# Kernel tuning notes

Hardware: AMD Instinct MI355X
Metric: run time of the kernel (lower is better)

## Reference

```python
import jax, jax.numpy as jnp
import numpy as np

N, E, H, C, G = 10000, 20000, 12, 768, 64  # nodes, edges, heads, per-head dim, graphs
NEG_SLOPE = 0.2


def _gat_layer(x, W, a_src, a_dst, b, src, dst):
    # x: [N, 768], W: [768, H*C], a_src/a_dst: [H, C], b: [C]
    h = (x @ W).reshape(-1, H, C)                      # [N, H, C]
    s = jnp.einsum('nhc,hc->nh', h, a_src)             # alpha_src per node
    d = jnp.einsum('nhc,hc->nh', h, a_dst)             # alpha_dst per node
    e = jax.nn.leaky_relu(s[src] + d[dst], NEG_SLOPE)  # [Etot, H]
    # segment softmax over incoming edges of each destination node
    m = jax.lax.stop_gradient(jax.ops.segment_max(e, dst, num_segments=N))
    ex = jnp.exp(e - m[dst])
    den = jax.ops.segment_sum(ex, dst, num_segments=N)
    alpha = ex / (den[dst] + 1e-16)                    # [Etot, H]
    out = jax.ops.segment_sum(h[src] * alpha[:, :, None], dst, num_segments=N)
    return out.mean(axis=1) + b                        # concat=False -> head mean, [N, C]


def setup_inputs() -> dict:
    key = jax.random.key(0)
    ks = jax.random.split(key, 16)
    sc = 0.02
    f32 = jnp.float32
    return {
        'x': jax.random.normal(ks[0], (N, 768), f32),
        'edge_index': jax.random.randint(ks[1], (2, E), 0, N),
        'batch': jnp.sort(jax.random.randint(ks[2], (N,), 0, G)),
        'W1': (jax.random.normal(ks[3], (768, H * C), f32) * sc),
        'a_src1': (jax.random.normal(ks[4], (H, C), f32) * sc),
        'a_dst1': (jax.random.normal(ks[5], (H, C), f32) * sc),
        'b1': jnp.zeros((C,), f32),
        'W2': (jax.random.normal(ks[6], (768, H * C), f32) * sc),
        'a_src2': (jax.random.normal(ks[7], (H, C), f32) * sc),
        'a_dst2': (jax.random.normal(ks[8], (H, C), f32) * sc),
        'b2': jnp.zeros((C,), f32),
        'mlp_w1': (jax.random.normal(ks[9], (768, 128), f32) * sc),
        'mlp_b1': jnp.zeros((128,), f32),
        'mlp_w2': (jax.random.normal(ks[10], (128, 4), f32) * sc),
        'mlp_b2': jnp.zeros((4,), f32),
    }


def reference(x, edge_index, batch, W1, a_src1, a_dst1, b1, W2, a_src2, a_dst2, b2,
              mlp_w1, mlp_b1, mlp_w2, mlp_b2):
    loops = jnp.arange(N)                               # GATConv add_self_loops=True
    src = jnp.concatenate([edge_index[0], loops])
    dst = jnp.concatenate([edge_index[1], loops])
    h = _gat_layer(x, W1, a_src1, a_dst1, b1, src, dst)
    h = _gat_layer(h, W2, a_src2, a_dst2, b2, src, dst)
    # scatter_mean over graph assignment
    ssum = jax.ops.segment_sum(h, batch, num_segments=G)
    cnt = jax.ops.segment_sum(jnp.ones((N,), h.dtype), batch, num_segments=G)
    g = ssum / jnp.maximum(cnt, 1.0)[:, None]           # [G, 768]
    z = jax.nn.relu(g @ mlp_w1 + mlp_b1)
    return z @ mlp_w2 + mlp_b2                          # [G, 4] logits
```

## Files before the change

### kernel.cpp

```cpp
#include <hip/hip_runtime.h>
#include <stdint.h>

typedef unsigned short u16;
typedef unsigned int   u32;

#define NNODES 10000
#define NEDGES 20000
#define ETOT   30000
#define NHEADS 12
#define CDIM   768
#define FDIM   768
#define KDIM   9216
#define NGRAPH 64
#define MPAD   10240
#define NEG_SLOPE 0.2f
#define DMAX   32

typedef __attribute__((ext_vector_type(8))) short short8;
typedef __attribute__((ext_vector_type(4))) float f32x4;

__device__ __forceinline__ u16 f32_bf16(float f) {
  u32 u = __float_as_uint(f);
  u = (u + 0x7FFFu + ((u >> 16) & 1u)) >> 16;
  return (u16)u;
}
__device__ __forceinline__ float bf16_f32(u16 v) {
  return __uint_as_float(((u32)v) << 16);
}

__global__ void k_count(const int* __restrict__ dste, int* __restrict__ counts) {
  int e = blockIdx.x * blockDim.x + threadIdx.x;
  if (e >= ETOT) return;
  int dst;
  if (e < NEDGES) dst = dste[e]; else dst = e - NEDGES;
  atomicAdd(&counts[dst], 1);
}

__global__ void k_scan(const int* __restrict__ counts, int* __restrict__ offs) {
  __shared__ int part[256];
  int t = threadIdx.x;
  const int chunk = 40;
  int beg = t * chunk;
  int end = beg + chunk; if (end > NNODES) end = NNODES;
  int s = 0;
  for (int i = beg; i < end && i < NNODES; i++) s += counts[i];
  part[t] = s;
  __syncthreads();
  for (int d = 1; d < 256; d <<= 1) {
    int v = (t >= d) ? part[t - d] : 0;
    __syncthreads();
    part[t] += v;
    __syncthreads();
  }
  int base = (t == 0) ? 0 : part[t - 1];
  for (int i = beg; i < end && i < NNODES; i++) { offs[i] = base; base += counts[i]; }
  if (t == 255) offs[NNODES] = base;
}

__global__ void k_seed(const int* __restrict__ offs, int* __restrict__ cursor) {
  int n = blockIdx.x * blockDim.x + threadIdx.x;
  if (n < NNODES) cursor[n] = offs[n];
}

__global__ void k_scatter(const int* __restrict__ dste, int* __restrict__ cursor,
                          int* __restrict__ elist) {
  int e = blockIdx.x * blockDim.x + threadIdx.x;
  if (e >= ETOT) return;
  int dst;
  if (e < NEDGES) dst = dste[e]; else dst = e - NEDGES;
  int pos = atomicAdd(&cursor[dst], 1);
  elist[pos] = e;
}

__global__ void k_U(const float* __restrict__ W, const float* __restrict__ a_src,
                    const float* __restrict__ a_dst, float* __restrict__ Ut) {
  int k = blockIdx.x;
  int t = threadIdx.x, w = t >> 6, l = t & 63;
  const float* Wrow = W + (size_t)k * KDIM;
#pragma unroll
  for (int q = 0; q < 6; q++) {
    int o = w * 6 + q;
    int h = (o < 12) ? o : o - 12;
    const float* av = (o < 12) ? (a_src + h * CDIM) : (a_dst + h * CDIM);
    const float* wr = Wrow + h * CDIM;
    float p = 0.f;
    for (int c = l; c < CDIM; c += 64) p += wr[c] * av[c];
#pragma unroll
    for (int d = 32; d > 0; d >>= 1) p += __shfl_down(p, d, 64);
    if (l == 0) Ut[o * FDIM + k] = p;
  }
}

__global__ void k_sd(const float* __restrict__ xin, const float* __restrict__ Ut,
                     float* __restrict__ sd, u16* __restrict__ xbf) {
  __shared__ float UtS[24 * FDIM];
  int t = threadIdx.x, w = t >> 6, l = t & 63;
  const float4* U4 = (const float4*)Ut;
  float4* S4 = (float4*)UtS;
  for (int i = t; i < 24 * FDIM / 4; i += 256) S4[i] = U4[i];
  __syncthreads();
#pragma unroll
  for (int rep = 0; rep < 5; rep++) {
    int n = blockIdx.x * 20 + w * 5 + rep;
    if (n >= NNODES) continue;
    const float* xr = xin + (size_t)n * FDIM;
    float4 x0 = *(const float4*)(xr + 4 * l);
    float4 x1 = *(const float4*)(xr + 4 * l + 256);
    float4 x2 = *(const float4*)(xr + 4 * l + 512);
    u16* xb = xbf + (size_t)n * FDIM + 4 * l;
    ushort4 p0, p1, p2;
    p0.x = f32_bf16(x0.x); p0.y = f32_bf16(x0.y); p0.z = f32_bf16(x0.z); p0.w = f32_bf16(x0.w);
    p1.x = f32_bf16(x1.x); p1.y = f32_bf16(x1.y); p1.z = f32_bf16(x1.z); p1.w = f32_bf16(x1.w);
    p2.x = f32_bf16(x2.x); p2.y = f32_bf16(x2.y); p2.z = f32_bf16(x2.z); p2.w = f32_bf16(x2.w);
    *(ushort4*)xb = p0;
    *(ushort4*)(xb + 256) = p1;
    *(ushort4*)(xb + 512) = p2;
#pragma unroll
    for (int o = 0; o < 24; o++) {
      const float4* up = (const float4*)(UtS + o * FDIM + 4 * l);
      float4 u0 = up[0];
      float4 u1 = up[64];
      float4 u2 = up[128];
      float a = x0.x * u0.x + x0.y * u0.y + x0.z * u0.z + x0.w * u0.w
              + x1.x * u1.x + x1.y * u1.y + x1.z * u1.z + x1.w * u1.w
              + x2.x * u2.x + x2.y * u2.y + x2.z * u2.z + x2.w * u2.w;
#pragma unroll
      for (int d = 32; d > 0; d >>= 1) a += __shfl_xor(a, d, 64);
      if (l == 0) sd[n * 24 + o] = a;
    }
  }
}

__global__ void k_trans(const float* __restrict__ W, u16* __restrict__ Bt) {
  int kt = blockIdx.x * 32, jt = blockIdx.y * 32;
  int tx = threadIdx.x, ty = threadIdx.y;
  __shared__ float tile[32][33];
#pragma unroll
  for (int r = 0; r < 4; r++)
    tile[ty + 8 * r][tx] = W[(size_t)(kt + ty + 8 * r) * KDIM + jt + tx];
  __syncthreads();
#pragma unroll
  for (int r = 0; r < 4; r++)
    Bt[(size_t)(jt + ty + 8 * r) * FDIM + kt + tx] = f32_bf16(tile[tx][ty + 8 * r]);
}

#define GLL16(G, L) __builtin_amdgcn_global_load_lds( \
  (const __attribute__((address_space(1))) void*)(G), \
  (__attribute__((address_space(3))) void*)(L), 16, 0, 0)

__global__ __launch_bounds__(512, 2) void k_gemm(const u16* __restrict__ A,
    const u16* __restrict__ B, u16* __restrict__ C) {
  __shared__ __align__(16) u16 As[2][256 * 64];
  __shared__ __align__(16) u16 Bs[2][256 * 64];
  int t = threadIdx.x;
  int w = t >> 6, l = t & 63;
  int swz = (blockIdx.x & 7) * 180 + (blockIdx.x >> 3);
  int by = swz / 36, bx = swz - by * 36;
  int row0 = by * 256, col0 = bx * 256;
  int wr = w >> 2, wc = w & 3;
  int lr = l & 15;
  int koff = (l >> 4) * 16;
  int swzr = (lr & 7) << 4;
  int rb = t >> 3;
  int csw = ((t & 7) ^ (rb & 7)) * 8;
  const u16* baseA = A + (size_t)(row0 + rb) * FDIM + csw;
  const u16* baseB = B + (size_t)(col0 + rb) * FDIM + csw;

  f32x4 acc[8][4] = {};
  short8 a[4][2], b0[2][2], b1[2][2];

  auto stA = [&](int buf, int h, int s) {
    const u16* g = baseA + (size_t)(h * 128) * FDIM + s * 64;
    u16* lp = (u16*)&As[buf][0] + h * 8192 + (w << 9);
    GLL16(g, lp);
    GLL16(g + (size_t)64 * FDIM, lp + 4096);
  };
  auto stB = [&](int buf, int h, int s) {
    const u16* g = baseB + (size_t)(h * 128) * FDIM + s * 64;
    u16* lp = (u16*)&Bs[buf][0] + h * 8192 + (w << 9);
    GLL16(g, lp);
    GLL16(g + (size_t)64 * FDIM, lp + 4096);
  };
  auto ldA = [&](int buf, int mo) {
#pragma unroll
    for (int m = 0; m < 4; m++)
#pragma unroll
      for (int c = 0; c < 2; c++) {
        int row = wr * 128 + (mo + m) * 16 + lr;
        int off = row * 128 + ((c * 64 + koff) ^ swzr);
        a[m][c] = *(const short8*)((const char*)&As[buf][0] + off);
      }
  };
  auto ldB = [&](int buf, short8 (*bb)[2], int no) {
#pragma unroll
    for (int n = 0; n < 2; n++)
#pragma unroll
      for (int c = 0; c < 2; c++) {
        int row = wc * 64 + (no + n) * 16 + lr;
        int off = row * 128 + ((c * 64 + koff) ^ swzr);
        bb[n][c] = *(const short8*)((const char*)&Bs[buf][0] + off);
      }
  };
  auto mm8 = [&](short8 (*bb)[2], int mo, int no) {
    __builtin_amdgcn_s_setprio(1);
#pragma unroll
    for (int m = 0; m < 4; m++)
#pragma unroll
      for (int n = 0; n < 2; n++)
#pragma unroll
        for (int c = 0; c < 2; c++)
          acc[mo + m][no + n] = __builtin_amdgcn_mfma_f32_16x16x32_bf16(
              a[m][c], bb[n][c], acc[mo + m][no + n], 0, 0, 0);
    __builtin_amdgcn_s_setprio(0);
  };

  stA(0, 0, 0); stA(0, 1, 0); stB(0, 0, 0); stB(0, 1, 0);
  stB(1, 0, 1); stA(1, 0, 1);
  asm volatile("s_waitcnt vmcnt(4)" ::: "memory");
  __builtin_amdgcn_s_barrier();

#pragma unroll
  for (int s = 0; s < 12; s++) {
    int P = s & 1;
    ldA(P, 0); ldB(P, b0, 0);
    if (s + 1 < 12) stB(P ^ 1, 1, s + 1);
    __builtin_amdgcn_s_barrier();
    mm8(b0, 0, 0);
    __builtin_amdgcn_s_barrier();
    ldB(P, b1, 2);
    if (s + 1 < 12) stA(P ^ 1, 1, s + 1);
    __builtin_amdgcn_s_barrier();
    mm8(b1, 0, 2);
    __builtin_amdgcn_s_barrier();
    ldA(P, 4);
    if (s + 2 < 12) stB(P, 0, s + 2);
    __builtin_amdgcn_s_barrier();
    mm8(b1, 4, 2);
    __builtin_amdgcn_s_barrier();
    if (s + 2 < 12) stA(P, 0, s + 2);
    __builtin_amdgcn_s_barrier();
    mm8(b0, 4, 0);
    if (s < 11) {
      if (s <= 9) asm volatile("s_waitcnt vmcnt(4)" ::: "memory");
      else        asm volatile("s_waitcnt vmcnt(0)" ::: "memory");
    }
    __builtin_amdgcn_s_barrier();
  }

  int lg = l >> 4;
#pragma unroll
  for (int m = 0; m < 8; m++)
#pragma unroll
    for (int n = 0; n < 4; n++) {
      int col = col0 + wc * 64 + n * 16 + lr;
#pragma unroll
      for (int r = 0; r < 4; r++) {
        int row = row0 + wr * 128 + m * 16 + lg * 4 + r;
        C[(size_t)row * KDIM + col] = f32_bf16(acc[m][n][r]);
      }
    }
}

__global__ void k_att(const u16* __restrict__ Hbig, const int* __restrict__ ei,
                      const int* __restrict__ offs, const int* __restrict__ elist,
                      const float* __restrict__ sd, const float* __restrict__ bias,
                      float* __restrict__ out) {
  int t = threadIdx.x, w = t >> 6, l = t & 63;
  int n = blockIdx.x * 4 + w;
  __shared__ int   srcsS[4][DMAX];
  __shared__ float alphS[4][NHEADS * DMAX];
  if (n >= NNODES) return;
  int* srcs = srcsS[w];
  float* alph = alphS[w];
  int beg = offs[n];
  int deg = offs[n + 1] - beg;
  if (deg > DMAX) deg = DMAX;
  if (l < deg) {
    int e = elist[beg + l];
    srcs[l] = (e < NEDGES) ? ei[e] : e - NEDGES;
  }
  __builtin_amdgcn_wave_barrier();
  for (int p = l; p < deg * NHEADS; p += 64) {
    int i = p / NHEADS, h = p - i * NHEADS;
    float v = sd[srcs[i] * 24 + h] + sd[n * 24 + 12 + h];
    v = (v > 0.f) ? v : NEG_SLOPE * v;
    alph[h * DMAX + i] = v;
  }
  __builtin_amdgcn_wave_barrier();
  if (l < NHEADS) {
    float m = -1e30f;
    for (int i = 0; i < deg; i++) m = fmaxf(m, alph[l * DMAX + i]);
    float s = 0.f;
    for (int i = 0; i < deg; i++) {
      float ex = expf(alph[l * DMAX + i] - m);
      alph[l * DMAX + i] = ex;
      s += ex;
    }
    float inv = 1.f / (s + 1e-16f);
    for (int i = 0; i < deg; i++) alph[l * DMAX + i] *= inv;
  }
  __builtin_amdgcn_wave_barrier();
#pragma unroll
  for (int pass = 0; pass < 3; pass++) {
    float4 acc = make_float4(0.f, 0.f, 0.f, 0.f);
    for (int i = 0; i < deg; i++) {
      const u16* hb = Hbig + (size_t)srcs[i] * KDIM + pass * 256 + 4 * l;
#pragma unroll
      for (int h = 0; h < NHEADS; h++) {
        ushort4 hv = *(const ushort4*)(hb + h * CDIM);
        float a = alph[h * DMAX + i];
        acc.x += a * bf16_f32(hv.x);
        acc.y += a * bf16_f32(hv.y);
        acc.z += a * bf16_f32(hv.z);
        acc.w += a * bf16_f32(hv.w);
      }
    }
    int c = pass * 256 + 4 * l;
    const float sc = 1.f / 12.f;
    float4 ov;
    ov.x = acc.x * sc + bias[c + 0];
    ov.y = acc.y * sc + bias[c + 1];
    ov.z = acc.z * sc + bias[c + 2];
    ov.w = acc.w * sc + bias[c + 3];
    *(float4*)(out + (size_t)n * FDIM + c) = ov;
  }
}

__global__ void k_pool(const float* __restrict__ h2, const int* __restrict__ batch,
                       float* __restrict__ g) {
  int gi = blockIdx.x;
  int c = blockIdx.y * 256 + threadIdx.x;
  int lo = 0, hi = NNODES;
  while (lo < hi) { int mid = (lo + hi) >> 1; if (batch[mid] < gi) lo = mid + 1; else hi = mid; }
  int start = lo;
  lo = start; hi = NNODES;
  while (lo < hi) { int mid = (lo + hi) >> 1; if (batch[mid] < gi + 1) lo = mid + 1; else hi = mid; }
  int end = lo;
  int cnt = end - start; if (cnt < 1) cnt = 1;
  float inv = 1.f / (float)cnt;
  float s = 0.f;
  for (int n = start; n < end; n++) s += h2[(size_t)n * FDIM + c];
  g[gi * FDIM + c] = s * inv;
}

__global__ void k_mlp(const float* __restrict__ g, const float* __restrict__ w1,
                      const float* __restrict__ b1, const float* __restrict__ w2,
                      const float* __restrict__ b2, float* __restrict__ out) {
  int gi = blockIdx.x;
  int t = threadIdx.x;
  __shared__ float gs[FDIM];
  __shared__ float zs[128];
  for (int i = t; i < FDIM; i += 128) gs[i] = g[gi * FDIM + i];
  __syncthreads();
  float a = b1[t];
  for (int k = 0; k < FDIM; k++) a += gs[k] * w1[k * 128 + t];
  zs[t] = (a > 0.f) ? a : 0.f;
  __syncthreads();
  if (t < 4) {
    float o = b2[t];
    for (int i = 0; i < 128; i++) o += zs[i] * w2[i * 4 + t];
    out[gi * 4 + t] = o;
  }
}

extern "C" void kernel_launch(void* const* d_in, const int* in_sizes, int n_in,
                              void* d_out, int out_size, void* d_ws, size_t ws_size,
                              hipStream_t stream) {
  const float* x    = (const float*)d_in[0];
  const int*   ei   = (const int*)d_in[1];
  const int*   batch= (const int*)d_in[2];
  const float* W1   = (const float*)d_in[3];
  const float* as1  = (const float*)d_in[4];
  const float* ad1  = (const float*)d_in[5];
  const float* b1   = (const float*)d_in[6];
  const float* W2   = (const float*)d_in[7];
  const float* as2  = (const float*)d_in[8];
  const float* ad2  = (const float*)d_in[9];
  const float* b2   = (const float*)d_in[10];
  const float* mw1  = (const float*)d_in[11];
  const float* mb1  = (const float*)d_in[12];
  const float* mw2  = (const float*)d_in[13];
  const float* mb2  = (const float*)d_in[14];
  float* out = (float*)d_out;
  (void)in_sizes; (void)n_in; (void)out_size; (void)ws_size;

  char* wsb = (char*)d_ws;
  size_t off = 0;
  auto alloc = [&](size_t bytes) -> void* {
    void* p = wsb + off;
    off += (bytes + 255) & ~(size_t)255;
    return p;
  };
  u16*  Hbig   = (u16*)alloc((size_t)MPAD * KDIM * 2);
  u16*  Bt     = (u16*)alloc((size_t)KDIM * FDIM * 2);
  float* h1    = (float*)alloc((size_t)NNODES * FDIM * 4);
  float* h2    = (float*)alloc((size_t)NNODES * FDIM * 4);
  u16*  xbf    = (u16*)h2;
  float* sd    = (float*)alloc((size_t)NNODES * 24 * 4);
  float* Ut    = (float*)alloc((size_t)FDIM * 24 * 4);
  int*  counts = (int*)alloc((size_t)NNODES * 4);
  int*  offs   = (int*)alloc((size_t)(NNODES + 1) * 4);
  int*  cursor = (int*)alloc((size_t)NNODES * 4);
  int*  elist  = (int*)alloc((size_t)ETOT * 4);
  float* gbuf  = (float*)alloc((size_t)NGRAPH * FDIM * 4);

  hipMemsetAsync(counts, 0, NNODES * 4, stream);
  hipMemsetAsync(xbf + (size_t)NNODES * FDIM, 0, (size_t)(MPAD - NNODES) * FDIM * 2, stream);
  k_count<<<(ETOT + 255) / 256, 256, 0, stream>>>(ei + NEDGES, counts);
  k_scan<<<1, 256, 0, stream>>>(counts, offs);
  k_seed<<<(NNODES + 255) / 256, 256, 0, stream>>>(offs, cursor);
  k_scatter<<<(ETOT + 255) / 256, 256, 0, stream>>>(ei + NEDGES, cursor, elist);

  for (int layer = 0; layer < 2; layer++) {
    const float* xin  = layer ? h1  : x;
    const float* W    = layer ? W2  : W1;
    const float* asrc = layer ? as2 : as1;
    const float* adst = layer ? ad2 : ad1;
    const float* bb   = layer ? b2  : b1;
    float* hout       = layer ? h2  : h1;

    k_U<<<FDIM, 256, 0, stream>>>(W, asrc, adst, Ut);
    k_sd<<<(NNODES + 19) / 20, 256, 0, stream>>>(xin, Ut, sd, xbf);
    k_trans<<<dim3(FDIM / 32, KDIM / 32), dim3(32, 8), 0, stream>>>(W, Bt);
    k_gemm<<<dim3((MPAD / 256) * (KDIM / 256)), 512, 0, stream>>>(xbf, Bt, Hbig);
    k_att<<<(NNODES + 3) / 4, 256, 0, stream>>>(Hbig, ei, offs, elist, sd, bb, hout);
  }

  k_pool<<<dim3(NGRAPH, 3), 256, 0, stream>>>(h2, batch, gbuf);
  k_mlp<<<NGRAPH, 128, 0, stream>>>(gbuf, mw1, mb1, mw2, mb2, out);
}
```

Before: 907.7 us.

## Aggregate raw features per head before projection, then GEMM with head-mean fused

The layer is reordered so that attention-weighted aggregation runs on the input features per head, producing a [N, 12*768] bf16 tensor, and the projection comes afterwards. The projection becomes one GEMM with K=9216 against a reshaped weight that sums over heads, and it fuses the 1/12 scale and the bias into its epilogue. This replaces the N×9216 output GEMM and the gather over the large H tensor with a 768-wide output. It relies on linearity and trades a larger bf16 intermediate write for less gather traffic and fewer output columns.

After: 876.9 us. 3.4% less time.

```diff
diff --git a/kernel.cpp b/kernel.cpp
--- a/kernel.cpp
+++ b/kernel.cpp
@@ -92,7 +92,7 @@
 }
 
 __global__ void k_sd(const float* __restrict__ xin, const float* __restrict__ Ut,
-                     float* __restrict__ sd, u16* __restrict__ xbf) {
+                     float* __restrict__ sd) {
   __shared__ float UtS[24 * FDIM];
   int t = threadIdx.x, w = t >> 6, l = t & 63;
   const float4* U4 = (const float4*)Ut;
@@ -107,14 +107,6 @@
     float4 x0 = *(const float4*)(xr + 4 * l);
     float4 x1 = *(const float4*)(xr + 4 * l + 256);
     float4 x2 = *(const float4*)(xr + 4 * l + 512);
-    u16* xb = xbf + (size_t)n * FDIM + 4 * l;
-    ushort4 p0, p1, p2;
-    p0.x = f32_bf16(x0.x); p0.y = f32_bf16(x0.y); p0.z = f32_bf16(x0.z); p0.w = f32_bf16(x0.w);
-    p1.x = f32_bf16(x1.x); p1.y = f32_bf16(x1.y); p1.z = f32_bf16(x1.z); p1.w = f32_bf16(x1.w);
-    p2.x = f32_bf16(x2.x); p2.y = f32_bf16(x2.y); p2.z = f32_bf16(x2.z); p2.w = f32_bf16(x2.w);
-    *(ushort4*)xb = p0;
-    *(ushort4*)(xb + 256) = p1;
-    *(ushort4*)(xb + 512) = p2;
 #pragma unroll
     for (int o = 0; o < 24; o++) {
       const float4* up = (const float4*)(UtS + o * FDIM + 4 * l);
@@ -131,140 +123,23 @@
   }
 }
 
-__global__ void k_trans(const float* __restrict__ W, u16* __restrict__ Bt) {
+__global__ void k_trans2(const float* __restrict__ W, u16* __restrict__ Bt2) {
   int kt = blockIdx.x * 32, jt = blockIdx.y * 32;
   int tx = threadIdx.x, ty = threadIdx.y;
   __shared__ float tile[32][33];
+  int h0 = jt / 768, c0 = jt - h0 * 768;
 #pragma unroll
   for (int r = 0; r < 4; r++)
     tile[ty + 8 * r][tx] = W[(size_t)(kt + ty + 8 * r) * KDIM + jt + tx];
   __syncthreads();
 #pragma unroll
   for (int r = 0; r < 4; r++)
-    Bt[(size_t)(jt + ty + 8 * r) * FDIM + kt + tx] = f32_bf16(tile[tx][ty + 8 * r]);
-}
-
-#define GLL16(G, L) __builtin_amdgcn_global_load_lds( \
-  (const __attribute__((address_space(1))) void*)(G), \
-  (__attribute__((address_space(3))) void*)(L), 16, 0, 0)
-
-__global__ __launch_bounds__(512, 2) void k_gemm(const u16* __restrict__ A,
-    const u16* __restrict__ B, u16* __restrict__ C) {
-  __shared__ __align__(16) u16 As[2][256 * 64];
-  __shared__ __align__(16) u16 Bs[2][256 * 64];
-  int t = threadIdx.x;
-  int w = t >> 6, l = t & 63;
-  int swz = (blockIdx.x & 7) * 180 + (blockIdx.x >> 3);
-  int by = swz / 36, bx = swz - by * 36;
-  int row0 = by * 256, col0 = bx * 256;
-  int wr = w >> 2, wc = w & 3;
-  int lr = l & 15;
-  int koff = (l >> 4) * 16;
-  int swzr = (lr & 7) << 4;
-  int rb = t >> 3;
-  int csw = ((t & 7) ^ (rb & 7)) * 8;
-  const u16* baseA = A + (size_t)(row0 + rb) * FDIM + csw;
-  const u16* baseB = B + (size_t)(col0 + rb) * FDIM + csw;
-
-  f32x4 acc[8][4] = {};
-  short8 a[4][2], b0[2][2], b1[2][2];
-
-  auto stA = [&](int buf, int h, int s) {
-    const u16* g = baseA + (size_t)(h * 128) * FDIM + s * 64;
-    u16* lp = (u16*)&As[buf][0] + h * 8192 + (w << 9);
-    GLL16(g, lp);
-    GLL16(g + (size_t)64 * FDIM, lp + 4096);
-  };
-  auto stB = [&](int buf, int h, int s) {
-    const u16* g = baseB + (size_t)(h * 128) * FDIM + s * 64;
-    u16* lp = (u16*)&Bs[buf][0] + h * 8192 + (w << 9);
-    GLL16(g, lp);
-    GLL16(g + (size_t)64 * FDIM, lp + 4096);
-  };
-  auto ldA = [&](int buf, int mo) {
-#pragma unroll
-    for (int m = 0; m < 4; m++)
-#pragma unroll
-      for (int c = 0; c < 2; c++) {
-        int row = wr * 128 + (mo + m) * 16 + lr;
-        int off = row * 128 + ((c * 64 + koff) ^ swzr);
-        a[m][c] = *(const short8*)((const char*)&As[buf][0] + off);
-      }
-  };
-  auto ldB = [&](int buf, short8 (*bb)[2], int no) {
-#pragma unroll
-    for (int n = 0; n < 2; n++)
-#pragma unroll
-      for (int c = 0; c < 2; c++) {
-        int row = wc * 64 + (no + n) * 16 + lr;
-        int off = row * 128 + ((c * 64 + koff) ^ swzr);
-        bb[n][c] = *(const short8*)((const char*)&Bs[buf][0] + off);
-      }
-  };
-  auto mm8 = [&](short8 (*bb)[2], int mo, int no) {
-    __builtin_amdgcn_s_setprio(1);
-#pragma unroll
-    for (int m = 0; m < 4; m++)
-#pragma unroll
-      for (int n = 0; n < 2; n++)
-#pragma unroll
-        for (int c = 0; c < 2; c++)
-          acc[mo + m][no + n] = __builtin_amdgcn_mfma_f32_16x16x32_bf16(
-              a[m][c], bb[n][c], acc[mo + m][no + n], 0, 0, 0);
-    __builtin_amdgcn_s_setprio(0);
-  };
-
-  stA(0, 0, 0); stA(0, 1, 0); stB(0, 0, 0); stB(0, 1, 0);
-  stB(1, 0, 1); stA(1, 0, 1);
-  asm volatile("s_waitcnt vmcnt(4)" ::: "memory");
-  __builtin_amdgcn_s_barrier();
-
-#pragma unroll
-  for (int s = 0; s < 12; s++) {
-    int P = s & 1;
-    ldA(P, 0); ldB(P, b0, 0);
-    if (s + 1 < 12) stB(P ^ 1, 1, s + 1);
-    __builtin_amdgcn_s_barrier();
-    mm8(b0, 0, 0);
-    __builtin_amdgcn_s_barrier();
-    ldB(P, b1, 2);
-    if (s + 1 < 12) stA(P ^ 1, 1, s + 1);
-    __builtin_amdgcn_s_barrier();
-    mm8(b1, 0, 2);
-    __builtin_amdgcn_s_barrier();
-    ldA(P, 4);
-    if (s + 2 < 12) stB(P, 0, s + 2);
-    __builtin_amdgcn_s_barrier();
-    mm8(b1, 4, 2);
-    __builtin_amdgcn_s_barrier();
-    if (s + 2 < 12) stA(P, 0, s + 2);
-    __builtin_amdgcn_s_barrier();
-    mm8(b0, 4, 0);
-    if (s < 11) {
-      if (s <= 9) asm volatile("s_waitcnt vmcnt(4)" ::: "memory");
-      else        asm volatile("s_waitcnt vmcnt(0)" ::: "memory");
-    }
-    __builtin_amdgcn_s_barrier();
-  }
-
-  int lg = l >> 4;
-#pragma unroll
-  for (int m = 0; m < 8; m++)
-#pragma unroll
-    for (int n = 0; n < 4; n++) {
-      int col = col0 + wc * 64 + n * 16 + lr;
-#pragma unroll
-      for (int r = 0; r < 4; r++) {
-        int row = row0 + wr * 128 + m * 16 + lg * 4 + r;
-        C[(size_t)row * KDIM + col] = f32_bf16(acc[m][n][r]);
-      }
-    }
-}
-
-__global__ void k_att(const u16* __restrict__ Hbig, const int* __restrict__ ei,
+    Bt2[(size_t)(c0 + ty + 8 * r) * KDIM + h0 * 768 + kt + tx] = f32_bf16(tile[tx][ty + 8 * r]);
+}
+
+__global__ void k_agg(const float* __restrict__ xin, const int* __restrict__ ei,
                       const int* __restrict__ offs, const int* __restrict__ elist,
-                      const float* __restrict__ sd, const float* __restrict__ bias,
-                      float* __restrict__ out) {
+                      const float* __restrict__ sd, u16* __restrict__ y) {
   int t = threadIdx.x, w = t >> 6, l = t & 63;
   int n = blockIdx.x * 4 + w;
   __shared__ int   srcsS[4][DMAX];
@@ -302,28 +177,160 @@
   __builtin_amdgcn_wave_barrier();
 #pragma unroll
   for (int pass = 0; pass < 3; pass++) {
-    float4 acc = make_float4(0.f, 0.f, 0.f, 0.f);
+    float4 acc12[NHEADS];
+#pragma unroll
+    for (int h = 0; h < NHEADS; h++) acc12[h] = make_float4(0.f, 0.f, 0.f, 0.f);
     for (int i = 0; i < deg; i++) {
-      const u16* hb = Hbig + (size_t)srcs[i] * KDIM + pass * 256 + 4 * l;
+      float4 xs = *(const float4*)(xin + (size_t)srcs[i] * FDIM + pass * 256 + 4 * l);
 #pragma unroll
       for (int h = 0; h < NHEADS; h++) {
-        ushort4 hv = *(const ushort4*)(hb + h * CDIM);
         float a = alph[h * DMAX + i];
-        acc.x += a * bf16_f32(hv.x);
-        acc.y += a * bf16_f32(hv.y);
-        acc.z += a * bf16_f32(hv.z);
-        acc.w += a * bf16_f32(hv.w);
+        acc12[h].x += a * xs.x;
+        acc12[h].y += a * xs.y;
+        acc12[h].z += a * xs.z;
+        acc12[h].w += a * xs.w;
       }
     }
-    int c = pass * 256 + 4 * l;
-    const float sc = 1.f / 12.f;
-    float4 ov;
-    ov.x = acc.x * sc + bias[c + 0];
-    ov.y = acc.y * sc + bias[c + 1];
-    ov.z = acc.z * sc + bias[c + 2];
-    ov.w = acc.w * sc + bias[c + 3];
-    *(float4*)(out + (size_t)n * FDIM + c) = ov;
-  }
+    u16* yr = y + (size_t)n * KDIM + pass * 256 + 4 * l;
+#pragma unroll
+    for (int h = 0; h < NHEADS; h++) {
+      ushort4 pv;
+      pv.x = f32_bf16(acc12[h].x);
+      pv.y = f32_bf16(acc12[h].y);
+      pv.z = f32_bf16(acc12[h].z);
+      pv.w = f32_bf16(acc12[h].w);
+      *(ushort4*)(yr + h * CDIM) = pv;
+    }
+  }
+}
+
+#define GLL16(G, L) __builtin_amdgcn_global_load_lds( \
+  (const __attribute__((address_space(1))) void*)(G), \
+  (__attribute__((address_space(3))) void*)(L), 16, 0, 0)
+
+__global__ __launch_bounds__(512, 2) void k_gemm2(const u16* __restrict__ A,
+    const u16* __restrict__ B, float* __restrict__ C, const float* __restrict__ bias) {
+  __shared__ __align__(16) u16 As[2][128 * 64];
+  __shared__ __align__(16) u16 Bs[2][256 * 64];
+  int t = threadIdx.x;
+  int w = t >> 6, l = t & 63;
+  int bid = blockIdx.x;
+  int xcd = bid & 7, j = bid >> 3;
+  int by = xcd * 10 + j / 3, bx = j % 3;
+  int row0 = by * 128, col0 = bx * 256;
+  int wr = w >> 2, wc = w & 3;
+  int lr = l & 15;
+  int koff = (l >> 4) * 16;
+  int swzr = (lr & 7) << 4;
+  int rb = t >> 3;
+  int csw = ((t & 7) ^ (rb & 7)) * 8;
+  const u16* baseA = A + (size_t)(row0 + rb) * KDIM + csw;
+  const u16* baseB = B + (size_t)(col0 + rb) * KDIM + csw;
+
+  f32x4 acc[4][4] = {};
+  short8 alo[2][2], ahi[2][2], blo[2][2], bhi[2][2];
+
+  auto stA2 = [&](int buf, int h, int s) {
+    const u16* g = baseA + (size_t)(h * 64) * KDIM + s * 64;
+    GLL16(g, (u16*)&As[buf][0] + h * 4096 + t * 8);
+  };
+  auto stB2 = [&](int buf, int h, int s) {
+    const u16* g = baseB + (size_t)(h * 128) * KDIM + s * 64;
+    u16* lp = (u16*)&Bs[buf][0] + h * 8192;
+    GLL16(g, lp + t * 8);
+    GLL16(g + (size_t)64 * KDIM, lp + 4096 + t * 8);
+  };
+  auto ldA2 = [&](int buf, short8 (*dst)[2], int mo) {
+#pragma unroll
+    for (int m = 0; m < 2; m++)
+#pragma unroll
+      for (int c = 0; c < 2; c++) {
+        int row = wr * 64 + (mo + m) * 16 + lr;
+        int off = row * 128 + ((c * 64 + koff) ^ swzr);
+        dst[m][c] = *(const short8*)((const char*)&As[buf][0] + off);
+      }
+  };
+  auto ldB2 = [&](int buf, short8 (*dst)[2], int no) {
+#pragma unroll
+    for (int n = 0; n < 2; n++)
+#pragma unroll
+      for (int c = 0; c < 2; c++) {
+        int row = wc * 64 + (no + n) * 16 + lr;
+        int off = row * 128 + ((c * 64 + koff) ^ swzr);
+        dst[n][c] = *(const short8*)((const char*)&Bs[buf][0] + off);
+      }
+  };
+  auto mm8 = [&](short8 (*aa)[2], short8 (*bb)[2], int mo, int no) {
+    __builtin_amdgcn_s_setprio(1);
+#pragma unroll
+    for (int m = 0; m < 2; m++)
+#pragma unroll
+      for (int n = 0; n < 2; n++)
+#pragma unroll
+        for (int c = 0; c < 2; c++)
+          acc[mo + m][no + n] = __builtin_amdgcn_mfma_f32_16x16x32_bf16(
+              aa[m][c], bb[n][c], acc[mo + m][no + n], 0, 0, 0);
+    __builtin_amdgcn_s_setprio(0);
+  };
+
+#define BAR() __builtin_amdgcn_s_barrier()
+#define TILE_STEADY(S, P) do { \
+    ldA2(P, alo, 0); ldB2(P, blo, 0); stB2((P) ^ 1, 1, (S) + 1); \
+    BAR(); mm8(alo, blo, 0, 0); BAR(); \
+    ldB2(P, bhi, 2); stA2((P) ^ 1, 1, (S) + 1); \
+    BAR(); mm8(alo, bhi, 0, 2); BAR(); \
+    ldA2(P, ahi, 2); stB2(P, 0, (S) + 2); \
+    BAR(); mm8(ahi, bhi, 2, 2); BAR(); \
+    stA2(P, 0, (S) + 2); \
+    BAR(); mm8(ahi, blo, 2, 0); \
+    asm volatile("s_waitcnt vmcnt(3)" ::: "memory"); \
+    BAR(); \
+  } while (0)
+
+  stB2(0, 0, 0); stB2(0, 1, 0); stA2(0, 0, 0); stA2(0, 1, 0);
+  stB2(1, 0, 1); stA2(1, 0, 1);
+  asm volatile("s_waitcnt vmcnt(3)" ::: "memory");
+  BAR();
+
+  const int NIT = KDIM / 64;
+  for (int s = 0; s < NIT - 2; s += 2) {
+    TILE_STEADY(s, 0);
+    TILE_STEADY(s + 1, 1);
+  }
+  ldA2(0, alo, 0); ldB2(0, blo, 0); stB2(1, 1, NIT - 1);
+  BAR(); mm8(alo, blo, 0, 0); BAR();
+  ldB2(0, bhi, 2); stA2(1, 1, NIT - 1);
+  BAR(); mm8(alo, bhi, 0, 2); BAR();
+  ldA2(0, ahi, 2);
+  BAR(); mm8(ahi, bhi, 2, 2); BAR();
+  BAR(); mm8(ahi, blo, 2, 0);
+  asm volatile("s_waitcnt vmcnt(0)" ::: "memory");
+  BAR();
+  ldA2(1, alo, 0); ldB2(1, blo, 0);
+  BAR(); mm8(alo, blo, 0, 0); BAR();
+  ldB2(1, bhi, 2);
+  BAR(); mm8(alo, bhi, 0, 2); BAR();
+  ldA2(1, ahi, 2);
+  BAR(); mm8(ahi, bhi, 2, 2); BAR();
+  mm8(ahi, blo, 2, 0);
+#undef TILE_STEADY
+#undef BAR
+
+  int lg = l >> 4;
+  const float sc = 1.f / 12.f;
+#pragma unroll
+  for (int m = 0; m < 4; m++)
+#pragma unroll
+    for (int n = 0; n < 4; n++) {
+      int col = col0 + wc * 64 + n * 16 + lr;
+      float bv = bias[col];
+#pragma unroll
+      for (int r = 0; r < 4; r++) {
+        int row = row0 + wr * 64 + m * 16 + lg * 4 + r;
+        if (row < NNODES)
+          C[(size_t)row * FDIM + col] = acc[m][n][r] * sc + bv;
+      }
+    }
 }
 
 __global__ void k_pool(const float* __restrict__ h2, const int* __restrict__ batch,
@@ -391,11 +398,10 @@
     off += (bytes + 255) & ~(size_t)255;
     return p;
   };
-  u16*  Hbig   = (u16*)alloc((size_t)MPAD * KDIM * 2);
-  u16*  Bt     = (u16*)alloc((size_t)KDIM * FDIM * 2);
+  u16*  y      = (u16*)alloc((size_t)MPAD * KDIM * 2);
+  u16*  Bt2    = (u16*)alloc((size_t)FDIM * KDIM * 2);
   float* h1    = (float*)alloc((size_t)NNODES * FDIM * 4);
   float* h2    = (float*)alloc((size_t)NNODES * FDIM * 4);
-  u16*  xbf    = (u16*)h2;
   float* sd    = (float*)alloc((size_t)NNODES * 24 * 4);
   float* Ut    = (float*)alloc((size_t)FDIM * 24 * 4);
   int*  counts = (int*)alloc((size_t)NNODES * 4);
@@ -405,7 +411,7 @@
   float* gbuf  = (float*)alloc((size_t)NGRAPH * FDIM * 4);
 
   hipMemsetAsync(counts, 0, NNODES * 4, stream);
-  hipMemsetAsync(xbf + (size_t)NNODES * FDIM, 0, (size_t)(MPAD - NNODES) * FDIM * 2, stream);
+  hipMemsetAsync(y + (size_t)NNODES * KDIM, 0, (size_t)(MPAD - NNODES) * KDIM * 2, stream);
   k_count<<<(ETOT + 255) / 256, 256, 0, stream>>>(ei + NEDGES, counts);
   k_scan<<<1, 256, 0, stream>>>(counts, offs);
   k_seed<<<(NNODES + 255) / 256, 256, 0, stream>>>(offs, cursor);
@@ -420,10 +426,10 @@
     float* hout       = layer ? h2  : h1;
 
     k_U<<<FDIM, 256, 0, stream>>>(W, asrc, adst, Ut);
-    k_sd<<<(NNODES + 19) / 20, 256, 0, stream>>>(xin, Ut, sd, xbf);
-    k_trans<<<dim3(FDIM / 32, KDIM / 32), dim3(32, 8), 0, stream>>>(W, Bt);
-    k_gemm<<<dim3((MPAD / 256) * (KDIM / 256)), 512, 0, stream>>>(xbf, Bt, Hbig);
-    k_att<<<(NNODES + 3) / 4, 256, 0, stream>>>(Hbig, ei, offs, elist, sd, bb, hout);
+    k_sd<<<(NNODES + 19) / 20, 256, 0, stream>>>(xin, Ut, sd);
+    k_trans2<<<dim3(FDIM / 32, KDIM / 32), dim3(32, 8), 0, stream>>>(W, Bt2);
+    k_agg<<<(NNODES + 3) / 4, 256, 0, stream>>>(xin, ei, offs, elist, sd, y);
+    k_gemm2<<<(MPAD / 128) * 3, 512, 0, stream>>>(y, Bt2, hout, bb);
   }
 
   k_pool<<<dim3(NGRAPH, 3), 256, 0, stream>>>(h2, batch, gbuf);
```

## Aggregate inputs over edges before projecting with a split-K GEMM

Applied to the files above, without the earlier changes.

Uses linearity to reorder each GAT layer: attention-weighted neighbour features are summed per head first (y = sum alpha·x_src, one 12×768 row per node), and the projection by W is applied afterwards as one K=9216 GEMM. The 18 KB-per-edge gather of the large projected tensor is replaced by a 3 KB-per-edge gather of fp32 input rows. Output is summed over heads directly inside the GEMM. The new GEMM has only 120 output tiles, so it splits K in two and adds a reduction kernel that also applies the 1/12 and bias. The y intermediate is still a large bf16 write, and the GEMM grid of 240 blocks may leave some CUs underused.

Result: no change. 894.8 us (-1.4%).

```diff
diff --git a/kernel.cpp b/kernel.cpp
--- a/kernel.cpp
+++ b/kernel.cpp
@@ -92,7 +92,7 @@
 }
 
 __global__ void k_sd(const float* __restrict__ xin, const float* __restrict__ Ut,
-                     float* __restrict__ sd, u16* __restrict__ xbf) {
+                     float* __restrict__ sd) {
   __shared__ float UtS[24 * FDIM];
   int t = threadIdx.x, w = t >> 6, l = t & 63;
   const float4* U4 = (const float4*)Ut;
@@ -107,14 +107,6 @@
     float4 x0 = *(const float4*)(xr + 4 * l);
     float4 x1 = *(const float4*)(xr + 4 * l + 256);
     float4 x2 = *(const float4*)(xr + 4 * l + 512);
-    u16* xb = xbf + (size_t)n * FDIM + 4 * l;
-    ushort4 p0, p1, p2;
-    p0.x = f32_bf16(x0.x); p0.y = f32_bf16(x0.y); p0.z = f32_bf16(x0.z); p0.w = f32_bf16(x0.w);
-    p1.x = f32_bf16(x1.x); p1.y = f32_bf16(x1.y); p1.z = f32_bf16(x1.z); p1.w = f32_bf16(x1.w);
-    p2.x = f32_bf16(x2.x); p2.y = f32_bf16(x2.y); p2.z = f32_bf16(x2.z); p2.w = f32_bf16(x2.w);
-    *(ushort4*)xb = p0;
-    *(ushort4*)(xb + 256) = p1;
-    *(ushort4*)(xb + 512) = p2;
 #pragma unroll
     for (int o = 0; o < 24; o++) {
       const float4* up = (const float4*)(UtS + o * FDIM + 4 * l);
@@ -131,140 +123,23 @@
   }
 }
 
-__global__ void k_trans(const float* __restrict__ W, u16* __restrict__ Bt) {
+__global__ void k_trans2(const float* __restrict__ W, u16* __restrict__ Bt2) {
   int kt = blockIdx.x * 32, jt = blockIdx.y * 32;
   int tx = threadIdx.x, ty = threadIdx.y;
   __shared__ float tile[32][33];
+  int h0 = jt / 768, c0 = jt - h0 * 768;
 #pragma unroll
   for (int r = 0; r < 4; r++)
     tile[ty + 8 * r][tx] = W[(size_t)(kt + ty + 8 * r) * KDIM + jt + tx];
   __syncthreads();
 #pragma unroll
   for (int r = 0; r < 4; r++)
-    Bt[(size_t)(jt + ty + 8 * r) * FDIM + kt + tx] = f32_bf16(tile[tx][ty + 8 * r]);
-}
-
-#define GLL16(G, L) __builtin_amdgcn_global_load_lds( \
-  (const __attribute__((address_space(1))) void*)(G), \
-  (__attribute__((address_space(3))) void*)(L), 16, 0, 0)
-
-__global__ __launch_bounds__(512, 2) void k_gemm(const u16* __restrict__ A,
-    const u16* __restrict__ B, u16* __restrict__ C) {
-  __shared__ __align__(16) u16 As[2][256 * 64];
-  __shared__ __align__(16) u16 Bs[2][256 * 64];
-  int t = threadIdx.x;
-  int w = t >> 6, l = t & 63;
-  int swz = (blockIdx.x & 7) * 180 + (blockIdx.x >> 3);
-  int by = swz / 36, bx = swz - by * 36;
-  int row0 = by * 256, col0 = bx * 256;
-  int wr = w >> 2, wc = w & 3;
-  int lr = l & 15;
-  int koff = (l >> 4) * 16;
-  int swzr = (lr & 7) << 4;
-  int rb = t >> 3;
-  int csw = ((t & 7) ^ (rb & 7)) * 8;
-  const u16* baseA = A + (size_t)(row0 + rb) * FDIM + csw;
-  const u16* baseB = B + (size_t)(col0 + rb) * FDIM + csw;
-
-  f32x4 acc[8][4] = {};
-  short8 a[4][2], b0[2][2], b1[2][2];
-
-  auto stA = [&](int buf, int h, int s) {
-    const u16* g = baseA + (size_t)(h * 128) * FDIM + s * 64;
-    u16* lp = (u16*)&As[buf][0] + h * 8192 + (w << 9);
-    GLL16(g, lp);
-    GLL16(g + (size_t)64 * FDIM, lp + 4096);
-  };
-  auto stB = [&](int buf, int h, int s) {
-    const u16* g = baseB + (size_t)(h * 128) * FDIM + s * 64;
-    u16* lp = (u16*)&Bs[buf][0] + h * 8192 + (w << 9);
-    GLL16(g, lp);
-    GLL16(g + (size_t)64 * FDIM, lp + 4096);
-  };
-  auto ldA = [&](int buf, int mo) {
-#pragma unroll
-    for (int m = 0; m < 4; m++)
-#pragma unroll
-      for (int c = 0; c < 2; c++) {
-        int row = wr * 128 + (mo + m) * 16 + lr;
-        int off = row * 128 + ((c * 64 + koff) ^ swzr);
-        a[m][c] = *(const short8*)((const char*)&As[buf][0] + off);
-      }
-  };
-  auto ldB = [&](int buf, short8 (*bb)[2], int no) {
-#pragma unroll
-    for (int n = 0; n < 2; n++)
-#pragma unroll
-      for (int c = 0; c < 2; c++) {
-        int row = wc * 64 + (no + n) * 16 + lr;
-        int off = row * 128 + ((c * 64 + koff) ^ swzr);
-        bb[n][c] = *(const short8*)((const char*)&Bs[buf][0] + off);
-      }
-  };
-  auto mm8 = [&](short8 (*bb)[2], int mo, int no) {
-    __builtin_amdgcn_s_setprio(1);
-#pragma unroll
-    for (int m = 0; m < 4; m++)
-#pragma unroll
-      for (int n = 0; n < 2; n++)
-#pragma unroll
-        for (int c = 0; c < 2; c++)
-          acc[mo + m][no + n] = __builtin_amdgcn_mfma_f32_16x16x32_bf16(
-              a[m][c], bb[n][c], acc[mo + m][no + n], 0, 0, 0);
-    __builtin_amdgcn_s_setprio(0);
-  };
-
-  stA(0, 0, 0); stA(0, 1, 0); stB(0, 0, 0); stB(0, 1, 0);
-  stB(1, 0, 1); stA(1, 0, 1);
-  asm volatile("s_waitcnt vmcnt(4)" ::: "memory");
-  __builtin_amdgcn_s_barrier();
-
-#pragma unroll
-  for (int s = 0; s < 12; s++) {
-    int P = s & 1;
-    ldA(P, 0); ldB(P, b0, 0);
-    if (s + 1 < 12) stB(P ^ 1, 1, s + 1);
-    __builtin_amdgcn_s_barrier();
-    mm8(b0, 0, 0);
-    __builtin_amdgcn_s_barrier();
-    ldB(P, b1, 2);
-    if (s + 1 < 12) stA(P ^ 1, 1, s + 1);
-    __builtin_amdgcn_s_barrier();
-    mm8(b1, 0, 2);
-    __builtin_amdgcn_s_barrier();
-    ldA(P, 4);
-    if (s + 2 < 12) stB(P, 0, s + 2);
-    __builtin_amdgcn_s_barrier();
-    mm8(b1, 4, 2);
-    __builtin_amdgcn_s_barrier();
-    if (s + 2 < 12) stA(P, 0, s + 2);
-    __builtin_amdgcn_s_barrier();
-    mm8(b0, 4, 0);
-    if (s < 11) {
-      if (s <= 9) asm volatile("s_waitcnt vmcnt(4)" ::: "memory");
-      else        asm volatile("s_waitcnt vmcnt(0)" ::: "memory");
-    }
-    __builtin_amdgcn_s_barrier();
-  }
-
-  int lg = l >> 4;
-#pragma unroll
-  for (int m = 0; m < 8; m++)
-#pragma unroll
-    for (int n = 0; n < 4; n++) {
-      int col = col0 + wc * 64 + n * 16 + lr;
-#pragma unroll
-      for (int r = 0; r < 4; r++) {
-        int row = row0 + wr * 128 + m * 16 + lg * 4 + r;
-        C[(size_t)row * KDIM + col] = f32_bf16(acc[m][n][r]);
-      }
-    }
-}
-
-__global__ void k_att(const u16* __restrict__ Hbig, const int* __restrict__ ei,
+    Bt2[(size_t)(c0 + ty + 8 * r) * KDIM + h0 * 768 + kt + tx] = f32_bf16(tile[tx][ty + 8 * r]);
+}
+
+__global__ void k_agg(const float* __restrict__ xin, const int* __restrict__ ei,
                       const int* __restrict__ offs, const int* __restrict__ elist,
-                      const float* __restrict__ sd, const float* __restrict__ bias,
-                      float* __restrict__ out) {
+                      const float* __restrict__ sd, u16* __restrict__ y) {
   int t = threadIdx.x, w = t >> 6, l = t & 63;
   int n = blockIdx.x * 4 + w;
   __shared__ int   srcsS[4][DMAX];
@@ -302,28 +177,169 @@
   __builtin_amdgcn_wave_barrier();
 #pragma unroll
   for (int pass = 0; pass < 3; pass++) {
-    float4 acc = make_float4(0.f, 0.f, 0.f, 0.f);
+    float4 acc12[NHEADS];
+#pragma unroll
+    for (int h = 0; h < NHEADS; h++) acc12[h] = make_float4(0.f, 0.f, 0.f, 0.f);
     for (int i = 0; i < deg; i++) {
-      const u16* hb = Hbig + (size_t)srcs[i] * KDIM + pass * 256 + 4 * l;
+      float4 xs = *(const float4*)(xin + (size_t)srcs[i] * FDIM + pass * 256 + 4 * l);
 #pragma unroll
       for (int h = 0; h < NHEADS; h++) {
-        ushort4 hv = *(const ushort4*)(hb + h * CDIM);
         float a = alph[h * DMAX + i];
-        acc.x += a * bf16_f32(hv.x);
-        acc.y += a * bf16_f32(hv.y);
-        acc.z += a * bf16_f32(hv.z);
-        acc.w += a * bf16_f32(hv.w);
+        acc12[h].x += a * xs.x;
+        acc12[h].y += a * xs.y;
+        acc12[h].z += a * xs.z;
+        acc12[h].w += a * xs.w;
       }
     }
-    int c = pass * 256 + 4 * l;
-    const float sc = 1.f / 12.f;
-    float4 ov;
-    ov.x = acc.x * sc + bias[c + 0];
-    ov.y = acc.y * sc + bias[c + 1];
-    ov.z = acc.z * sc + bias[c + 2];
-    ov.w = acc.w * sc + bias[c + 3];
-    *(float4*)(out + (size_t)n * FDIM + c) = ov;
-  }
+    u16* yr = y + (size_t)n * KDIM + pass * 256 + 4 * l;
+#pragma unroll
+    for (int h = 0; h < NHEADS; h++) {
+      ushort4 pv;
+      pv.x = f32_bf16(acc12[h].x);
+      pv.y = f32_bf16(acc12[h].y);
+      pv.z = f32_bf16(acc12[h].z);
+      pv.w = f32_bf16(acc12[h].w);
+      *(ushort4*)(yr + h * CDIM) = pv;
+    }
+  }
+}
+
+#define GLL16(G, L) __builtin_amdgcn_global_load_lds( \
+  (const __attribute__((address_space(1))) void*)(G), \
+  (__attribute__((address_space(3))) void*)(L), 16, 0, 0)
+
+__global__ __launch_bounds__(512, 2) void k_gemm2(const u16* __restrict__ A,
+    const u16* __restrict__ B, float* __restrict__ C0, float* __restrict__ C1) {
+  __shared__ __align__(16) u16 As[2][256 * 64];
+  __shared__ __align__(16) u16 Bs[2][256 * 64];
+  int t = threadIdx.x;
+  int w = t >> 6, l = t & 63;
+  int bid = blockIdx.x;
+  int xcd = bid & 7, j = bid >> 3;
+  int p = j / 6, rem = j - p * 6;
+  int ks = rem / 3, cx = rem - ks * 3;
+  int by = xcd * 5 + p;
+  int row0 = by * 256, col0 = cx * 256;
+  int kbase = ks * (KDIM / 2);
+  int wr = w >> 2, wc = w & 3;
+  int lr = l & 15;
+  int koff = (l >> 4) * 16;
+  int swzr = (lr & 7) << 4;
+  int rb = t >> 3;
+  int csw = ((t & 7) ^ (rb & 7)) * 8;
+  const u16* baseA = A + (size_t)(row0 + rb) * KDIM + kbase + csw;
+  const u16* baseB = B + (size_t)(col0 + rb) * KDIM + kbase + csw;
+
+  f32x4 acc[8][4] = {};
+  short8 a[4][2], b0[2][2], b1[2][2];
+
+  auto stA = [&](int buf, int h, int s) {
+    const u16* g = baseA + (size_t)(h * 128) * KDIM + s * 64;
+    u16* lp = (u16*)&As[buf][0] + h * 8192 + (w << 9);
+    GLL16(g, lp);
+    GLL16(g + (size_t)64 * KDIM, lp + 4096);
+  };
+  auto stB = [&](int buf, int h, int s) {
+    const u16* g = baseB + (size_t)(h * 128) * KDIM + s * 64;
+    u16* lp = (u16*)&Bs[buf][0] + h * 8192 + (w << 9);
+    GLL16(g, lp);
+    GLL16(g + (size_t)64 * KDIM, lp + 4096);
+  };
+  auto ldA = [&](int buf, int mo) {
+#pragma unroll
+    for (int m = 0; m < 4; m++)
+#pragma unroll
+      for (int c = 0; c < 2; c++) {
+        int row = wr * 128 + (mo + m) * 16 + lr;
+        int off = row * 128 + ((c * 64 + koff) ^ swzr);
+        a[m][c] = *(const short8*)((const char*)&As[buf][0] + off);
+      }
+  };
+  auto ldB = [&](int buf, short8 (*bb)[2], int no) {
+#pragma unroll
+    for (int n = 0; n < 2; n++)
+#pragma unroll
+      for (int c = 0; c < 2; c++) {
+        int row = wc * 64 + (no + n) * 16 + lr;
+        int off = row * 128 + ((c * 64 + koff) ^ swzr);
+        bb[n][c] = *(const short8*)((const char*)&Bs[buf][0] + off);
+      }
+  };
+  auto mm8 = [&](short8 (*bb)[2], int mo, int no) {
+    __builtin_amdgcn_s_setprio(1);
+#pragma unroll
+    for (int m = 0; m < 4; m++)
+#pragma unroll
+      for (int n = 0; n < 2; n++)
+#pragma unroll
+        for (int c = 0; c < 2; c++)
+          acc[mo + m][no + n] = __builtin_amdgcn_mfma_f32_16x16x32_bf16(
+              a[m][c], bb[n][c], acc[mo + m][no + n], 0, 0, 0);
+    __builtin_amdgcn_s_setprio(0);
+  };
+
+  stA(0, 0, 0); stA(0, 1, 0); stB(0, 0, 0); stB(0, 1, 0);
+  stB(1, 0, 1); stA(1, 0, 1);
+  asm volatile("s_waitcnt vmcnt(4)" ::: "memory");
+  __builtin_amdgcn_s_barrier();
+
+  const int NIT = KDIM / 2 / 64;
+  for (int s = 0; s < NIT; s++) {
+    int P = s & 1;
+    ldA(P, 0); ldB(P, b0, 0);
+    if (s + 1 < NIT) stB(P ^ 1, 1, s + 1);
+    __builtin_amdgcn_s_barrier();
+    mm8(b0, 0, 0);
+    __builtin_amdgcn_s_barrier();
+    ldB(P, b1, 2);
+    if (s + 1 < NIT) stA(P ^ 1, 1, s + 1);
+    __builtin_amdgcn_s_barrier();
+    mm8(b1, 0, 2);
+    __builtin_amdgcn_s_barrier();
+    ldA(P, 4);
+    if (s + 2 < NIT) stB(P, 0, s + 2);
+    __builtin_amdgcn_s_barrier();
+    mm8(b1, 4, 2);
+    __builtin_amdgcn_s_barrier();
+    if (s + 2 < NIT) stA(P, 0, s + 2);
+    __builtin_amdgcn_s_barrier();
+    mm8(b0, 4, 0);
+    if (s < NIT - 1) {
+      if (s <= NIT - 3) asm volatile("s_waitcnt vmcnt(4)" ::: "memory");
+      else              asm volatile("s_waitcnt vmcnt(0)" ::: "memory");
+    }
+    __builtin_amdgcn_s_barrier();
+  }
+
+  float* Cd = ks ? C1 : C0;
+  int lg = l >> 4;
+#pragma unroll
+  for (int m = 0; m < 8; m++)
+#pragma unroll
+    for (int n = 0; n < 4; n++) {
+      int col = col0 + wc * 64 + n * 16 + lr;
+#pragma unroll
+      for (int r = 0; r < 4; r++) {
+        int row = row0 + wr * 128 + m * 16 + lg * 4 + r;
+        if (row < NNODES)
+          Cd[(size_t)row * FDIM + col] = acc[m][n][r];
+      }
+    }
+}
+
+__global__ void k_red(const float* __restrict__ p1, const float* __restrict__ bias,
+                      float* __restrict__ io) {
+  int e = (blockIdx.x * 256 + threadIdx.x) * 4;
+  float4 a = *(const float4*)(io + e);
+  float4 b = *(const float4*)(p1 + e);
+  float4 bv = *(const float4*)(bias + (e % FDIM));
+  const float sc = 1.f / 12.f;
+  float4 o;
+  o.x = (a.x + b.x) * sc + bv.x;
+  o.y = (a.y + b.y) * sc + bv.y;
+  o.z = (a.z + b.z) * sc + bv.z;
+  o.w = (a.w + b.w) * sc + bv.w;
+  *(float4*)(io + e) = o;
 }
 
 __global__ void k_pool(const float* __restrict__ h2, const int* __restrict__ batch,
@@ -391,11 +407,10 @@
     off += (bytes + 255) & ~(size_t)255;
     return p;
   };
-  u16*  Hbig   = (u16*)alloc((size_t)MPAD * KDIM * 2);
-  u16*  Bt     = (u16*)alloc((size_t)KDIM * FDIM * 2);
+  u16*  y      = (u16*)alloc((size_t)MPAD * KDIM * 2);
+  u16*  Bt2    = (u16*)alloc((size_t)FDIM * KDIM * 2);
   float* h1    = (float*)alloc((size_t)NNODES * FDIM * 4);
   float* h2    = (float*)alloc((size_t)NNODES * FDIM * 4);
-  u16*  xbf    = (u16*)h2;
   float* sd    = (float*)alloc((size_t)NNODES * 24 * 4);
   float* Ut    = (float*)alloc((size_t)FDIM * 24 * 4);
   int*  counts = (int*)alloc((size_t)NNODES * 4);
@@ -405,7 +420,7 @@
   float* gbuf  = (float*)alloc((size_t)NGRAPH * FDIM * 4);
 
   hipMemsetAsync(counts, 0, NNODES * 4, stream);
-  hipMemsetAsync(xbf + (size_t)NNODES * FDIM, 0, (size_t)(MPAD - NNODES) * FDIM * 2, stream);
+  hipMemsetAsync(y + (size_t)NNODES * KDIM, 0, (size_t)(MPAD - NNODES) * KDIM * 2, stream);
   k_count<<<(ETOT + 255) / 256, 256, 0, stream>>>(ei + NEDGES, counts);
   k_scan<<<1, 256, 0, stream>>>(counts, offs);
   k_seed<<<(NNODES + 255) / 256, 256, 0, stream>>>(offs, cursor);
@@ -418,12 +433,14 @@
     const float* adst = layer ? ad2 : ad1;
     const float* bb   = layer ? b2  : b1;
     float* hout       = layer ? h2  : h1;
+    float* cpart      = layer ? h1  : h2;
 
     k_U<<<FDIM, 256, 0, stream>>>(W, asrc, adst, Ut);
-    k_sd<<<(NNODES + 19) / 20, 256, 0, stream>>>(xin, Ut, sd, xbf);
-    k_trans<<<dim3(FDIM / 32, KDIM / 32), dim3(32, 8), 0, stream>>>(W, Bt);
-    k_gemm<<<dim3((MPAD / 256) * (KDIM / 256)), 512, 0, stream>>>(xbf, Bt, Hbig);
-    k_att<<<(NNODES + 3) / 4, 256, 0, stream>>>(Hbig, ei, offs, elist, sd, bb, hout);
+    k_sd<<<(NNODES + 19) / 20, 256, 0, stream>>>(xin, Ut, sd);
+    k_trans2<<<dim3(FDIM / 32, KDIM / 32), dim3(32, 8), 0, stream>>>(W, Bt2);
+    k_agg<<<(NNODES + 3) / 4, 256, 0, stream>>>(xin, ei, offs, elist, sd, y);
+    k_gemm2<<<240, 512, 0, stream>>>(y, Bt2, hout, cpart);
+    k_red<<<NNODES * FDIM / 1024, 256, 0, stream>>>(cpart, bb, hout);
   }
 
   k_pool<<<dim3(NGRAPH, 3), 256, 0, stream>>>(h2, batch, gbuf);
```
